# Kernel tuning notes

Measured on AMD Instinct MI355X. Metric: run time of the kernel, lower is better.

## Reference

```python
import jax, jax.numpy as jnp
import numpy as np

OC, IC, K, STRIDE, PAD, DIL, GROUPS = 256, 256, 3, 1, 1, 1, 1


def _conv_one(x, w):
    # x: [C, H, W], w: [OC, IC//groups, K, K]
    out = jax.lax.conv_general_dilated(
        x[None], w,
        window_strides=(STRIDE, STRIDE),
        padding=[(PAD, PAD), (PAD, PAD)],
        rhs_dilation=(DIL, DIL),
        dimension_numbers=("NCHW", "OIHW", "NCHW"),
        feature_group_count=GROUPS,
    )
    return out[0]  # [OC, H', W']


def setup_inputs() -> dict:
    key = jax.random.key(0)
    k1, k2, k3, k4 = jax.random.split(key, 4)
    B, num = 32, 64
    inputs = jax.random.normal(k1, (B, IC, 56, 56), dtype=jnp.float32)
    inputs_se = jax.random.normal(k2, (B, num), dtype=jnp.float32)
    fan = IC * K * K
    weight = jax.random.normal(k3, (OC * IC * K * K // GROUPS, num), dtype=jnp.float32) / np.sqrt(num * fan)
    bias = jax.random.normal(k4, (OC,), dtype=jnp.float32) * 0.01
    return {"inputs": inputs, "inputs_se": inputs_se, "weight": weight, "bias": bias}


def reference(inputs, inputs_se, weight, bias):
    B = inputs.shape[0]
    # per-sample weight synthesis: [B, OC*IC*K*K//groups]
    w = jnp.einsum("bn,on->bo", inputs_se, weight)
    w = w.reshape(B, OC, IC // GROUPS, K, K)
    out = jax.vmap(_conv_one)(inputs, w)  # [B, OC, H', W']
    return out + bias.reshape(1, -1, 1, 1)
```

## Files before the change

### kernel.cpp

```cpp
#include <hip/hip_runtime.h>

typedef __bf16 bf16x8 __attribute__((ext_vector_type(8)));
typedef float  f32x4  __attribute__((ext_vector_type(4)));

#define B_   32
#define OC   256
#define IC   256
#define HW   3136
#define HP   60
#define WP   58
#define KTOT 2304
#define NT   36
#define XPAD_BYTES ((size_t)B_ * HP * WP * IC * 2)

__device__ __forceinline__ void async16(const void* g, void* l) {
    __builtin_amdgcn_global_load_lds(
        (__attribute__((address_space(1))) void*)g,
        (__attribute__((address_space(3))) void*)l, 16, 0, 0);
}

__global__ __launch_bounds__(256) void zero_border(__bf16* __restrict__ Xpad) {
    int t   = blockIdx.x * 256 + threadIdx.x;
    int b   = t / 11008;
    int r2  = t - b * 11008;
    int pos = r2 >> 5, iq = r2 & 31;
    int r, c;
    if (pos < 232) { int rr = pos / 58; c = pos - rr * 58; r = (rr == 0) ? 0 : (56 + rr); }
    else           { int p2 = pos - 232; r = 1 + (p2 >> 1); c = (p2 & 1) * 57; }
    uint4 z = make_uint4(0u, 0u, 0u, 0u);
    *(uint4*)(Xpad + ((size_t)b * (HP * WP) + r * WP + c) * IC + iq * 8) = z;
}

__global__ __launch_bounds__(256) void transpose_pad(
    const float* __restrict__ X, __bf16* __restrict__ Xpad) {
    int sc = blockIdx.x, icc = blockIdx.y, b = blockIdx.z;
    __shared__ float lt[64][65];
    int tid = threadIdx.x;
    {
        int ci = tid >> 2, sq = tid & 3;
        const float* src = X + (size_t)(b * IC + icc * 64 + ci) * HW + sc * 64 + sq * 16;
        float4 v0 = ((const float4*)src)[0];
        float4 v1 = ((const float4*)src)[1];
        float4 v2 = ((const float4*)src)[2];
        float4 v3 = ((const float4*)src)[3];
        float* dst = &lt[ci][sq * 16];
        ((float4*)dst)[0] = v0; ((float4*)dst)[1] = v1;
        ((float4*)dst)[2] = v2; ((float4*)dst)[3] = v3;
    }
    __syncthreads();
    {
        int p = tid >> 2, iq = tid & 3;
        int s = sc * 64 + p;
        int h = s / 56, w = s - h * 56;
        __bf16* dst = Xpad + ((size_t)b * (HP * WP) + (h + 1) * WP + (w + 1)) * IC + icc * 64 + iq * 16;
        bf16x8 v0, v1;
        #pragma unroll
        for (int j = 0; j < 8; ++j) v0[j] = (__bf16)lt[iq * 16 + j][p];
        #pragma unroll
        for (int j = 0; j < 8; ++j) v1[j] = (__bf16)lt[iq * 16 + 8 + j][p];
        *(bf16x8*)dst = v0;
        *(bf16x8*)(dst + 8) = v1;
    }
}

__global__ __launch_bounds__(256) void synth(
    const float* __restrict__ se, const float* __restrict__ weight,
    __bf16* __restrict__ Asyn) {
    int oc = blockIdx.x / 9, tap = blockIdx.x - oc * 9;
    int tid = threadIdx.x;
    const float* wrow = weight + ((size_t)(oc * 256 + tid) * 9 + tap) * 64;
    float4 w[16];
    #pragma unroll
    for (int i = 0; i < 16; ++i) w[i] = ((const float4*)wrow)[i];
    size_t outb = (size_t)oc * KTOT + tap * 256 + tid;
    #pragma unroll
    for (int b = 0; b < 32; ++b) {
        const float4* sb = (const float4*)(se + b * 64);
        float acc = 0.f;
        #pragma unroll
        for (int i = 0; i < 16; ++i) {
            float4 s4 = sb[i];
            acc += w[i].x * s4.x + w[i].y * s4.y + w[i].z * s4.z + w[i].w * s4.w;
        }
        Asyn[(size_t)b * OC * KTOT + outb] = (__bf16)acc;
    }
}

__global__ __launch_bounds__(512, 2) void conv_mfma(
    const __bf16* __restrict__ Asyn, const __bf16* __restrict__ Xpad,
    const float* __restrict__ bias, float* __restrict__ Out) {
    const int i = blockIdx.x;
    const int xcd = i & 7, slot = i >> 3;
    const int bg = slot / 13, ntile = slot - bg * 13;
    const int b = xcd + 8 * bg;

    __shared__ __bf16 Al[2][256 * 64];
    __shared__ __bf16 Bl[2][256 * 64];

    const int tid = threadIdx.x;
    const int wid = tid >> 6, lane = tid & 63;

    const int rsub = lane >> 3;
    const int q = (lane & 7) ^ rsub;
    const int rowA0 = wid * 32 + rsub;
    const __bf16* aptr = Asyn + (size_t)(b * OC + rowA0) * KTOT + q * 8;
    const __bf16* xb = Xpad + (size_t)b * (HP * WP) * IC;
    const __bf16* bptr[4];
    #pragma unroll
    for (int c = 0; c < 4; ++c) {
        int nn = ntile * 256 + wid * 32 + c * 8 + rsub;
        if (nn >= HW) nn -= HW;
        const int h = nn / 56, w = nn - h * 56;
        bptr[c] = xb + (h * WP + w) * IC + q * 8;
    }

    const int wm = wid >> 2;
    const int wn = wid & 3;
    const int fr = lane & 15, fq = lane >> 4;
    const int swz = (fq ^ (fr & 7)) * 16;
    const int abase = (wm * 128 + fr) * 128 + swz;
    const int bbase = (wn * 64 + fr) * 128 + swz;

    f32x4 acc[8][4] = {};

    auto STAGE = [&](int t, int s) {
        const int tap = t >> 2, sub = t & 3;
        const int kh = (tap * 11) >> 5;
        const int kw = tap - kh * 3;
        const int aoK = t * 64;
        const int boK = (kh * WP + kw) * IC + sub * 64;
        char* al = (char*)&Al[s][0] + wid * 4096;
        char* bl = (char*)&Bl[s][0] + wid * 4096;
        #pragma unroll
        for (int c = 0; c < 4; ++c)
            async16(aptr + (size_t)c * (8 * KTOT) + aoK, al + c * 1024);
        #pragma unroll
        for (int c = 0; c < 4; ++c)
            async16(bptr[c] + boK, bl + c * 1024);
    };

    auto COMPUTE = [&](int s) {
        const char* Ab = (const char*)&Al[s][0];
        const char* Bb = (const char*)&Bl[s][0];
        bf16x8 bv[4][2];
        #pragma unroll
        for (int ni = 0; ni < 4; ++ni)
            #pragma unroll
            for (int tt = 0; tt < 2; ++tt)
                bv[ni][tt] = *(const bf16x8*)(Bb + ((bbase + ni * 2048) ^ (tt * 64)));
        #pragma unroll
        for (int p = 0; p < 4; ++p) {
            bf16x8 af[2][2];
            #pragma unroll
            for (int m2 = 0; m2 < 2; ++m2)
                #pragma unroll
                for (int tt = 0; tt < 2; ++tt)
                    af[m2][tt] = *(const bf16x8*)(Ab + ((abase + (2 * p + m2) * 2048) ^ (tt * 64)));
            __builtin_amdgcn_s_setprio(1);
            #pragma unroll
            for (int m2 = 0; m2 < 2; ++m2)
                #pragma unroll
                for (int ni = 0; ni < 4; ++ni) {
                    acc[2 * p + m2][ni] = __builtin_amdgcn_mfma_f32_16x16x32_bf16(
                        af[m2][0], bv[ni][0], acc[2 * p + m2][ni], 0, 0, 0);
                    acc[2 * p + m2][ni] = __builtin_amdgcn_mfma_f32_16x16x32_bf16(
                        af[m2][1], bv[ni][1], acc[2 * p + m2][ni], 0, 0, 0);
                }
            __builtin_amdgcn_s_setprio(0);
        }
    };

    STAGE(0, 0);
    #pragma unroll 2
    for (int t = 0; t < NT; ++t) {
        if (t + 1 < NT) {
            STAGE(t + 1, (t + 1) & 1);
            asm volatile("s_waitcnt vmcnt(8)" ::: "memory");
        } else {
            asm volatile("s_waitcnt vmcnt(0)" ::: "memory");
        }
        __builtin_amdgcn_s_barrier();
        asm volatile("" ::: "memory");
        COMPUTE(t & 1);
        asm volatile("" ::: "memory");
        __builtin_amdgcn_s_barrier();
        asm volatile("" ::: "memory");
    }

    #pragma unroll
    for (int mi = 0; mi < 8; ++mi) {
        #pragma unroll
        for (int r = 0; r < 4; ++r) {
            const int row = wm * 128 + mi * 16 + fq * 4 + r;
            const float bvv = bias[row];
            float* orow = Out + (size_t)(b * OC + row) * HW;
            #pragma unroll
            for (int ni = 0; ni < 4; ++ni) {
                const int col = ntile * 256 + wn * 64 + ni * 16 + fr;
                if (col < HW) orow[col] = acc[mi][ni][r] + bvv;
            }
        }
    }
}

extern "C" void kernel_launch(void* const* d_in, const int* in_sizes, int n_in,
                              void* d_out, int out_size, void* d_ws, size_t ws_size,
                              hipStream_t stream) {
    const float* X    = (const float*)d_in[0];
    const float* se   = (const float*)d_in[1];
    const float* Wt   = (const float*)d_in[2];
    const float* bias = (const float*)d_in[3];
    __bf16* Xpad = (__bf16*)d_ws;
    __bf16* Asyn = (__bf16*)((char*)d_ws + XPAD_BYTES);
    float*  Out  = (float*)d_out;

    zero_border<<<1376, 256, 0, stream>>>(Xpad);
    transpose_pad<<<dim3(49, 4, 32), 256, 0, stream>>>(X, Xpad);
    synth<<<2304, 256, 0, stream>>>(se, Wt, Asyn);
    conv_mfma<<<416, 512, 0, stream>>>(Asyn, Xpad, bias, Out);
}
```

Before: 509.5 us.

## Interleave split A/B async loads with MFMA phases in an 8-wave ping-pong schedule

Restructures the conv main loop so that A tiles are prefetched one step ahead and B tiles two steps ahead. The loads are split into halves and issued between the four MFMA sub-phases, with per-phase barriers and explicit vmcnt/lgkmcnt waits. This aims to hide global-to-LDS latency behind compute and to spread memory issue evenly, instead of issuing all loads at once before each tile. In exchange it adds many more barriers per tile and relies on a fragile LDS buffer-reuse ordering: B for t+2 is written into the buffer currently being read.

```diff
diff --git a/kernel.cpp b/kernel.cpp
--- a/kernel.cpp
+++ b/kernel.cpp
@@ -102,17 +102,20 @@
 
     const int rsub = lane >> 3;
     const int q = (lane & 7) ^ rsub;
-    const int rowA0 = wid * 32 + rsub;
-    const __bf16* aptr = Asyn + (size_t)(b * OC + rowA0) * KTOT + q * 8;
+    const __bf16* aptr[2][2];
+    const __bf16* bptr[2][2];
     const __bf16* xb = Xpad + (size_t)b * (HP * WP) * IC;
-    const __bf16* bptr[4];
-    #pragma unroll
-    for (int c = 0; c < 4; ++c) {
-        int nn = ntile * 256 + wid * 32 + c * 8 + rsub;
-        if (nn >= HW) nn -= HW;
-        const int h = nn / 56, w = nn - h * 56;
-        bptr[c] = xb + (h * WP + w) * IC + q * 8;
-    }
+    #pragma unroll
+    for (int h = 0; h < 2; ++h)
+        #pragma unroll
+        for (int c = 0; c < 2; ++c) {
+            const int r = h * 128 + wid * 16 + c * 8 + rsub;
+            aptr[h][c] = Asyn + (size_t)(b * OC + r) * KTOT + q * 8;
+            int nn = ntile * 256 + r;
+            if (nn >= HW) nn -= HW;
+            const int hh = nn / 56, ww = nn - hh * 56;
+            bptr[h][c] = xb + (hh * WP + ww) * IC + q * 8;
+        }
 
     const int wm = wid >> 2;
     const int wn = wid & 3;
@@ -123,68 +126,77 @@
 
     f32x4 acc[8][4] = {};
 
-    auto STAGE = [&](int t, int s) {
+    auto STAGE_A = [&](int t, int cur, int h) {
+        char* base = (char*)&Al[cur][0] + (h * 128 + wid * 16) * 128;
+        const int ko = t * 64;
+        async16(aptr[h][0] + ko, base);
+        async16(aptr[h][1] + ko, base + 1024);
+    };
+    auto STAGE_B = [&](int t, int cur, int h) {
         const int tap = t >> 2, sub = t & 3;
-        const int kh = (tap * 11) >> 5;
-        const int kw = tap - kh * 3;
-        const int aoK = t * 64;
-        const int boK = (kh * WP + kw) * IC + sub * 64;
-        char* al = (char*)&Al[s][0] + wid * 4096;
-        char* bl = (char*)&Bl[s][0] + wid * 4096;
-        #pragma unroll
-        for (int c = 0; c < 4; ++c)
-            async16(aptr + (size_t)c * (8 * KTOT) + aoK, al + c * 1024);
-        #pragma unroll
-        for (int c = 0; c < 4; ++c)
-            async16(bptr[c] + boK, bl + c * 1024);
+        const int kh = tap / 3, kw = tap - kh * 3;
+        const int ko = (kh * WP + kw) * IC + sub * 64;
+        char* base = (char*)&Bl[cur][0] + (h * 128 + wid * 16) * 128;
+        async16(bptr[h][0] + ko, base);
+        async16(bptr[h][1] + ko, base + 1024);
     };
 
-    auto COMPUTE = [&](int s) {
-        const char* Ab = (const char*)&Al[s][0];
-        const char* Bb = (const char*)&Bl[s][0];
+    auto TILE = [&](int t, int cur) {
+        const char* Ab = (const char*)&Al[cur][0];
+        const char* Bb = (const char*)&Bl[cur][0];
         bf16x8 bv[4][2];
         #pragma unroll
-        for (int ni = 0; ni < 4; ++ni)
-            #pragma unroll
-            for (int tt = 0; tt < 2; ++tt)
-                bv[ni][tt] = *(const bf16x8*)(Bb + ((bbase + ni * 2048) ^ (tt * 64)));
-        #pragma unroll
-        for (int p = 0; p < 4; ++p) {
+        for (int qq = 0; qq < 4; ++qq) {
+            if (qq == 0) {
+                #pragma unroll
+                for (int ni = 0; ni < 4; ++ni)
+                    #pragma unroll
+                    for (int tt = 0; tt < 2; ++tt)
+                        bv[ni][tt] = *(const bf16x8*)(Bb + ((bbase + ni * 2048) ^ (tt * 64)));
+            }
             bf16x8 af[2][2];
             #pragma unroll
             for (int m2 = 0; m2 < 2; ++m2)
                 #pragma unroll
                 for (int tt = 0; tt < 2; ++tt)
-                    af[m2][tt] = *(const bf16x8*)(Ab + ((abase + (2 * p + m2) * 2048) ^ (tt * 64)));
+                    af[m2][tt] = *(const bf16x8*)(Ab + ((abase + (2 * qq + m2) * 2048) ^ (tt * 64)));
+            if (qq == 0 && t + 1 < NT) STAGE_A(t + 1, cur ^ 1, 0);
+            if (qq == 1 && t + 1 < NT) STAGE_A(t + 1, cur ^ 1, 1);
+            if (qq == 2 && t + 2 < NT) STAGE_B(t + 2, cur, 0);
+            if (qq == 3) {
+                if (t + 2 < NT) STAGE_B(t + 2, cur, 1);
+                if (t < NT - 2) asm volatile("s_waitcnt vmcnt(4)" ::: "memory");
+                else            asm volatile("s_waitcnt vmcnt(0)" ::: "memory");
+            }
+            if (qq == 0) asm volatile("s_waitcnt lgkmcnt(8)" ::: "memory");
+            __builtin_amdgcn_s_barrier();
+            asm volatile("s_waitcnt lgkmcnt(0)" ::: "memory");
+            __builtin_amdgcn_sched_barrier(0);
             __builtin_amdgcn_s_setprio(1);
             #pragma unroll
             for (int m2 = 0; m2 < 2; ++m2)
                 #pragma unroll
                 for (int ni = 0; ni < 4; ++ni) {
-                    acc[2 * p + m2][ni] = __builtin_amdgcn_mfma_f32_16x16x32_bf16(
-                        af[m2][0], bv[ni][0], acc[2 * p + m2][ni], 0, 0, 0);
-                    acc[2 * p + m2][ni] = __builtin_amdgcn_mfma_f32_16x16x32_bf16(
-                        af[m2][1], bv[ni][1], acc[2 * p + m2][ni], 0, 0, 0);
+                    acc[2 * qq + m2][ni] = __builtin_amdgcn_mfma_f32_16x16x32_bf16(
+                        af[m2][0], bv[ni][0], acc[2 * qq + m2][ni], 0, 0, 0);
+                    acc[2 * qq + m2][ni] = __builtin_amdgcn_mfma_f32_16x16x32_bf16(
+                        af[m2][1], bv[ni][1], acc[2 * qq + m2][ni], 0, 0, 0);
                 }
             __builtin_amdgcn_s_setprio(0);
+            __builtin_amdgcn_s_barrier();
         }
     };
 
-    STAGE(0, 0);
-    #pragma unroll 2
-    for (int t = 0; t < NT; ++t) {
-        if (t + 1 < NT) {
-            STAGE(t + 1, (t + 1) & 1);
-            asm volatile("s_waitcnt vmcnt(8)" ::: "memory");
-        } else {
-            asm volatile("s_waitcnt vmcnt(0)" ::: "memory");
-        }
-        __builtin_amdgcn_s_barrier();
-        asm volatile("" ::: "memory");
-        COMPUTE(t & 1);
-        asm volatile("" ::: "memory");
-        __builtin_amdgcn_s_barrier();
-        asm volatile("" ::: "memory");
+    STAGE_A(0, 0, 0); STAGE_A(0, 0, 1);
+    STAGE_B(0, 0, 0); STAGE_B(0, 0, 1);
+    STAGE_B(1, 1, 0); STAGE_B(1, 1, 1);
+    asm volatile("s_waitcnt vmcnt(4)" ::: "memory");
+    __builtin_amdgcn_s_barrier();
+
+    #pragma unroll 1
+    for (int t2 = 0; t2 < NT; t2 += 2) {
+        TILE(t2, 0);
+        TILE(t2 + 1, 1);
     }
 
     #pragma unroll
```

Measured after the change: 489.5 us. -3.9%, faster.
